# Kernel tuning notes

Hardware: AMD Instinct MI355X
Metric: run time of the kernel (lower is better)

## Reference

```python
import jax, jax.numpy as jnp
import numpy as np

E = 1024
H = 16
D = E // H
NUM_BUCKETS = 320
MAX_DISTANCE = 800


def _relative_positions_bucket(relative_positions):
    # relative_positions: int32 [T, S]
    num_buckets = NUM_BUCKETS // 2  # 160
    relative_buckets = (relative_positions > 0).astype(jnp.int32) * num_buckets
    rel = jnp.abs(relative_positions)
    max_exact = num_buckets // 2  # 80
    is_small = rel < max_exact
    rel_f = jnp.maximum(rel, 1).astype(jnp.float32)
    large = jnp.log(rel_f / max_exact) / np.log(MAX_DISTANCE / max_exact) * (num_buckets - max_exact)
    large = (max_exact + large).astype(jnp.int32)
    large = jnp.minimum(large, num_buckets - 1)
    relative_buckets = relative_buckets + jnp.where(is_small, rel, large)
    return relative_buckets


def setup_inputs() -> dict:
    key = jax.random.key(0)
    ks = jax.random.split(key, 12)
    B, T = 2, 2048
    s = 0.02
    return {
        "hidden_states": jax.random.normal(ks[0], (B, T, E), dtype=jnp.float32),
        "q_w": jax.random.normal(ks[1], (E, E), dtype=jnp.float32) * s,
        "q_b": jnp.zeros((E,), dtype=jnp.float32),
        "k_w": jax.random.normal(ks[2], (E, E), dtype=jnp.float32) * s,
        "k_b": jnp.zeros((E,), dtype=jnp.float32),
        "v_w": jax.random.normal(ks[3], (E, E), dtype=jnp.float32) * s,
        "v_b": jnp.zeros((E,), dtype=jnp.float32),
        "out_w": jax.random.normal(ks[4], (E, E), dtype=jnp.float32) * s,
        "out_b": jnp.zeros((E,), dtype=jnp.float32),
        "rel_embed": jax.random.normal(ks[5], (NUM_BUCKETS, H), dtype=jnp.float32) * s,
        "gru_const": jnp.ones((1, H, 1, 1), dtype=jnp.float32),
        "gru_w": jax.random.normal(ks[6], (8, D), dtype=jnp.float32) * s,
        "gru_b": jnp.zeros((8,), dtype=jnp.float32),
    }


def reference(hidden_states, q_w, q_b, k_w, k_b, v_w, v_b, out_w, out_b,
              rel_embed, gru_const, gru_w, gru_b):
    B, T, _ = hidden_states.shape
    scaling = D ** (-0.5)

    # --- relative position bias: [H, T, T] ---
    ctx = jnp.arange(T, dtype=jnp.int32)[:, None]
    mem = jnp.arange(T, dtype=jnp.int32)[None, :]
    buckets = _relative_positions_bucket(mem - ctx)          # [T, T]
    position_bias = rel_embed[buckets]                        # [T, T, H]
    position_bias = jnp.transpose(position_bias, (2, 0, 1))   # [H, T, T]

    # --- gate (gru_rel_pos): per (b, h, t) scalar ---
    gated = hidden_states.reshape(B, T, H, D).transpose(0, 2, 1, 3)  # [B,H,T,D]
    proj = jnp.einsum('bhtd,ed->bhte', gated, gru_w) + gru_b         # [B,H,T,8]
    proj = proj.reshape(B, H, T, 2, 4).sum(-1)                        # [B,H,T,2]
    gate = jax.nn.sigmoid(proj)
    gate_a = gate[..., 0:1]
    gate_b = gate[..., 1:2]
    gate_out = gate_a * (gate_b * gru_const - 1.0) + 2.0              # [B,H,T,1]
    gated_position_bias = gate_out * position_bias[None]              # [B,H,T,T]

    # --- attention (same math as F.multi_head_attention_forward eager path) ---
    q = (hidden_states @ q_w.T + q_b).reshape(B, T, H, D).transpose(0, 2, 1, 3) * scaling
    k = (hidden_states @ k_w.T + k_b).reshape(B, T, H, D).transpose(0, 2, 1, 3)
    v = (hidden_states @ v_w.T + v_b).reshape(B, T, H, D).transpose(0, 2, 1, 3)

    scores = jnp.einsum('bhtd,bhsd->bhts', q, k) + gated_position_bias
    attn = jax.nn.softmax(scores, axis=-1)
    ctx_out = jnp.einsum('bhts,bhsd->bhtd', attn, v)                  # [B,H,T,D]
    ctx_out = ctx_out.transpose(0, 2, 1, 3).reshape(B, T, E)
    return ctx_out @ out_w.T + out_b
```

## Files before the change

kernel.cpp:

```cpp
#include <hip/hip_runtime.h>
#include <hip/hip_bf16.h>
#include <math.h>

typedef __bf16 bf16;
typedef __bf16 bf16x4 __attribute__((ext_vector_type(4)));
typedef __bf16 bf16x8 __attribute__((ext_vector_type(8)));
typedef float  f32x4  __attribute__((ext_vector_type(4)));

#define T_SEQ 2048
#define E_DIM 1024
#define H_NUM 16
#define D_DIM 64
#define NDELTA 4095
#define LOG2E 1.4426950408889634f

__device__ __forceinline__ void gld16(const bf16* g, bf16* l) {
  __builtin_amdgcn_global_load_lds((__attribute__((address_space(1))) void*)(g),
                                   (__attribute__((address_space(3))) void*)(l), 16, 0, 0);
}

__global__ void cast_bf16_kernel(const float* __restrict__ src, bf16* __restrict__ dst, int n4) {
  int i = blockIdx.x * blockDim.x + threadIdx.x;
  if (i >= n4) return;
  const float4 v = reinterpret_cast<const float4*>(src)[i];
  bf16x4 o;
  o[0] = (bf16)v.x; o[1] = (bf16)v.y; o[2] = (bf16)v.z; o[3] = (bf16)v.w;
  reinterpret_cast<bf16x4*>(dst)[i] = o;
}

__global__ void cast_w_kernel(const float* __restrict__ q_w, const float* __restrict__ k_w,
                              const float* __restrict__ v_w, const float* __restrict__ o_w,
                              bf16* __restrict__ wcat, bf16* __restrict__ wob) {
  int i = blockIdx.x * 256 + threadIdx.x;
  int sel = blockIdx.y;
  const float* src = (sel == 0) ? q_w : (sel == 1) ? k_w : (sel == 2) ? v_w : o_w;
  bf16* dst = (sel < 3) ? (wcat + (size_t)sel * 1048576) : wob;
  const float4 v = reinterpret_cast<const float4*>(src)[i];
  bf16x4 o;
  o[0] = (bf16)v.x; o[1] = (bf16)v.y; o[2] = (bf16)v.z; o[3] = (bf16)v.w;
  reinterpret_cast<bf16x4*>(dst)[i] = o;
}

__global__ void pb_kernel(const float* __restrict__ rel_embed, float* __restrict__ pbt) {
  int dd = blockIdx.x * 64 + threadIdx.x;
  if (dd >= NDELTA) return;
  int delta = dd - (T_SEQ - 1);
  int bucket = (delta > 0) ? 160 : 0;
  int rel = abs(delta);
  int v;
  if (rel < 80) {
    v = rel;
  } else {
    float rf = (float)(rel < 1 ? 1 : rel);
    float lf = logf(rf / 80.0f) * (80.0f / 2.302585092994046f);
    int lg = 80 + (int)lf;
    v = lg < 159 ? lg : 159;
  }
  bucket += v;
#pragma unroll
  for (int h = 0; h < H_NUM; h++)
    pbt[h * NDELTA + dd] = rel_embed[bucket * H_NUM + h];
}

__global__ __launch_bounds__(256)
void gate_kernel(const float* __restrict__ hs, const float* __restrict__ gru_w,
                 const float* __restrict__ gru_b, const float* __restrict__ gconst,
                 float* __restrict__ gate)
{
  __shared__ float w[512];
  int tid = threadIdx.x;
  w[tid] = gru_w[tid];
  w[tid + 256] = gru_w[tid + 256];
  __syncthreads();
  int idx = blockIdx.x * 256 + tid;
  int h  = idx & 15;
  int bt = idx >> 4;
  const float* x = hs + (size_t)bt * E_DIM + h * D_DIM;
  float acc[8] = {0,0,0,0,0,0,0,0};
  for (int d = 0; d < 64; d += 4) {
    float4 xv = *(const float4*)&x[d];
#pragma unroll
    for (int e = 0; e < 8; e++) {
      acc[e] += xv.x * w[e*64+d] + xv.y * w[e*64+d+1]
              + xv.z * w[e*64+d+2] + xv.w * w[e*64+d+3];
    }
  }
  float p0 = acc[0]+acc[1]+acc[2]+acc[3] + gru_b[0]+gru_b[1]+gru_b[2]+gru_b[3];
  float p1 = acc[4]+acc[5]+acc[6]+acc[7] + gru_b[4]+gru_b[5]+gru_b[6]+gru_b[7];
  float ga = 1.0f / (1.0f + expf(-p0));
  float gb = 1.0f / (1.0f + expf(-p1));
  float g = (ga * (gb * gconst[h] - 1.0f) + 2.0f) * LOG2E;
  int bb = bt >> 11;
  int t  = bt & (T_SEQ - 1);
  gate[((size_t)(bb * H_NUM + h)) * T_SEQ + t] = g;
}

template<int MODE, int N_TOTAL>
__global__ __launch_bounds__(256)
void gemm2_kernel(const bf16* __restrict__ A, const bf16* __restrict__ W,
                  const float* __restrict__ b0, const float* __restrict__ b1,
                  const float* __restrict__ b2, float qalpha,
                  void* __restrict__ out0, void* __restrict__ out1, void* __restrict__ out2)
{
  __shared__ bf16 As[128 * 32];
  __shared__ bf16 Bs[128 * 32];
  const int tid  = threadIdx.x;
  const int lane = tid & 63;
  const int wave = tid >> 6;
  const int m0 = blockIdx.y * 128;
  const int n0 = blockIdx.x * 128;
  const int wm = (wave >> 1) * 64;
  const int wn = (wave & 1) * 64;
  const int qd = lane >> 4;
  const int lm = lane & 15;

  const int row4 = lane >> 2;
  const int col8 = (lane & 3) * 8;
  const bf16* gA0 = A + (size_t)(m0 + wave * 32 + row4) * 1024 + col8;
  const bf16* gA1 = gA0 + (size_t)16 * 1024;
  const bf16* gB0 = W + (size_t)(n0 + wave * 32 + row4) * 1024 + col8;
  const bf16* gB1 = gB0 + (size_t)16 * 1024;
  bf16* lA0 = As + (wave * 2 + 0) * 512;
  bf16* lA1 = As + (wave * 2 + 1) * 512;
  bf16* lB0 = Bs + (wave * 2 + 0) * 512;
  bf16* lB1 = Bs + (wave * 2 + 1) * 512;

  f32x4 acc[4][4] = {};

  for (int k0 = 0; k0 < 1024; k0 += 32) {
    gld16(gA0 + k0, lA0);
    gld16(gA1 + k0, lA1);
    gld16(gB0 + k0, lB0);
    gld16(gB1 + k0, lB1);
    __syncthreads();
    bf16x8 af[4], bfr[4];
#pragma unroll
    for (int i = 0; i < 4; i++) {
      af[i]  = *(const bf16x8*)&As[(wm + i * 16 + lm) * 32 + qd * 8];
      bfr[i] = *(const bf16x8*)&Bs[(wn + i * 16 + lm) * 32 + qd * 8];
    }
#pragma unroll
    for (int im = 0; im < 4; im++)
#pragma unroll
      for (int in = 0; in < 4; in++)
        acc[im][in] = __builtin_amdgcn_mfma_f32_16x16x32_bf16(af[im], bfr[in], acc[im][in], 0, 0, 0);
    __syncthreads();
  }

  const int seg = n0 >> 10;
  const float* bias = (MODE == 0) ? b0 : (seg == 0 ? b0 : (seg == 1 ? b1 : b2));
  const float alpha = (MODE == 1 && seg == 0) ? qalpha : 1.0f;

#pragma unroll
  for (int im = 0; im < 4; im++) {
#pragma unroll
    for (int in = 0; in < 4; in++) {
      const int n  = n0 + wn + in * 16 + lm;
      const int n1 = n & 1023;
      const float bv = bias[n1];
      const int mb = m0 + wm + im * 16 + qd * 4;
      if (MODE == 0) {
        float* o = (float*)out0;
#pragma unroll
        for (int r = 0; r < 4; r++)
          o[(size_t)(mb + r) * 1024 + n1] = acc[im][in][r] + bv;
      } else if (seg == 2) {
        const int bb = mb >> 11;
        const int t  = mb & 2047;
        bf16x4 pk;
#pragma unroll
        for (int r = 0; r < 4; r++) pk[r] = (bf16)(acc[im][in][r] + bv);
        *(bf16x4*)&((bf16*)out2)[((size_t)(bb * 1024 + n1)) * 2048 + t] = pk;
      } else {
        bf16* o = (bf16*)(seg == 0 ? out0 : out1);
#pragma unroll
        for (int r = 0; r < 4; r++)
          o[(size_t)(mb + r) * 1024 + n1] = (bf16)((acc[im][in][r] + bv) * alpha);
      }
    }
  }
}

#define LK 72
__global__ __launch_bounds__(256)
void attn3_kernel(const bf16* __restrict__ Qg, const bf16* __restrict__ Kg,
                  const bf16* __restrict__ Vtg, const float* __restrict__ gate,
                  const float* __restrict__ pbt, bf16* __restrict__ ctx)
{
  __shared__ bf16 Ks[2][64 * LK];
  __shared__ bf16 Vs[2][64 * LK];
  __shared__ bf16 Ps[4][32 * LK];
  __shared__ float pbs[2176];

  const int t0 = blockIdx.x * 128;
  const int h  = blockIdx.y;
  const int b  = blockIdx.z;
  const int tid  = threadIdx.x;
  const int lane = tid & 63;
  const int wave = tid >> 6;
  const int qd = lane >> 4;
  const int lm = lane & 15;

  for (int i = tid; i < 2176; i += 256) {
    int idx = i - t0 + 1920;
    pbs[i] = (idx >= 0 && idx < NDELTA) ? pbt[h * NDELTA + idx] : 0.0f;
  }

  bf16x8 qf[2][2];
  float g[2];
#pragma unroll
  for (int nb = 0; nb < 2; nb++) {
    const int q = t0 + wave * 32 + nb * 16 + lm;
    const bf16* qrow = Qg + (size_t)(b * T_SEQ + q) * E_DIM + h * D_DIM;
    qf[nb][0] = *(const bf16x8*)(qrow + qd * 8);
    qf[nb][1] = *(const bf16x8*)(qrow + 32 + qd * 8);
    g[nb] = gate[((size_t)(b * H_NUM + h)) * T_SEQ + q];
  }

  const int srow = tid >> 2;
  const int scol = (tid & 3) * 16;
  const bf16* kgp = Kg  + ((size_t)(b * T_SEQ) + srow) * E_DIM + h * D_DIM + scol;
  const bf16* vgp = Vtg + ((size_t)(b * 1024) + h * D_DIM + srow) * T_SEQ + scol;

  {
    bf16x8 a0 = *(const bf16x8*)kgp;
    bf16x8 a1 = *(const bf16x8*)(kgp + 8);
    bf16x8 c0 = *(const bf16x8*)vgp;
    bf16x8 c1 = *(const bf16x8*)(vgp + 8);
    *(bf16x8*)&Ks[0][srow * LK + scol]     = a0;
    *(bf16x8*)&Ks[0][srow * LK + scol + 8] = a1;
    *(bf16x8*)&Vs[0][srow * LK + scol]     = c0;
    *(bf16x8*)&Vs[0][srow * LK + scol + 8] = c1;
  }
  __syncthreads();

  f32x4 o[4][2] = {};
  float li[2] = {0.0f, 0.0f};
  bf16* psw = &Ps[wave][0];

  for (int it = 0; it < T_SEQ / 64; it++) {
    const int s0 = it * 64;
    const int buf = it & 1;
    const bool more = (it + 1 < T_SEQ / 64);
    bf16x8 nk0, nk1, nv0, nv1;
    if (more) {
      const bf16* kn = kgp + (size_t)(s0 + 64) * E_DIM;
      const bf16* vn = vgp + (s0 + 64);
      nk0 = *(const bf16x8*)kn; nk1 = *(const bf16x8*)(kn + 8);
      nv0 = *(const bf16x8*)vn; nv1 = *(const bf16x8*)(vn + 8);
    }

    bf16x8 kf[4][2];
#pragma unroll
    for (int mb = 0; mb < 4; mb++) {
      kf[mb][0] = *(const bf16x8*)&Ks[buf][(16 * mb + lm) * LK + qd * 8];
      kf[mb][1] = *(const bf16x8*)&Ks[buf][(16 * mb + lm) * LK + 32 + qd * 8];
    }
#pragma unroll
    for (int nb = 0; nb < 2; nb++) {
      f32x4 sc[4];
#pragma unroll
      for (int mb = 0; mb < 4; mb++) {
        f32x4 t = {};
        t = __builtin_amdgcn_mfma_f32_16x16x32_bf16(kf[mb][0], qf[nb][0], t, 0, 0, 0);
        t = __builtin_amdgcn_mfma_f32_16x16x32_bf16(kf[mb][1], qf[nb][1], t, 0, 0, 0);
        sc[mb] = t;
      }
      const int ib = s0 + 4 * qd + 127 - (wave * 32 + nb * 16 + lm);
      float rs = 0.0f;
#pragma unroll
      for (int mb = 0; mb < 4; mb++) {
        bf16x4 pk;
#pragma unroll
        for (int r = 0; r < 4; r++) {
          float p = __builtin_amdgcn_exp2f(sc[mb][r] + g[nb] * pbs[ib + 16 * mb + r]);
          rs += p;
          pk[r] = (bf16)p;
        }
        *(bf16x4*)&psw[(nb * 16 + lm) * LK + 16 * mb + 4 * qd] = pk;
      }
      li[nb] += rs;
    }
    bf16x8 pf[2][2];
#pragma unroll
    for (int nb = 0; nb < 2; nb++) {
      pf[nb][0] = *(const bf16x8*)&psw[(nb * 16 + lm) * LK + qd * 8];
      pf[nb][1] = *(const bf16x8*)&psw[(nb * 16 + lm) * LK + 32 + qd * 8];
    }
#pragma unroll
    for (int db = 0; db < 4; db++) {
      bf16x8 vf0 = *(const bf16x8*)&Vs[buf][(16 * db + lm) * LK + qd * 8];
      bf16x8 vf1 = *(const bf16x8*)&Vs[buf][(16 * db + lm) * LK + 32 + qd * 8];
#pragma unroll
      for (int nb = 0; nb < 2; nb++) {
        o[db][nb] = __builtin_amdgcn_mfma_f32_16x16x32_bf16(vf0, pf[nb][0], o[db][nb], 0, 0, 0);
        o[db][nb] = __builtin_amdgcn_mfma_f32_16x16x32_bf16(vf1, pf[nb][1], o[db][nb], 0, 0, 0);
      }
    }
    if (more) {
      *(bf16x8*)&Ks[buf ^ 1][srow * LK + scol]     = nk0;
      *(bf16x8*)&Ks[buf ^ 1][srow * LK + scol + 8] = nk1;
      *(bf16x8*)&Vs[buf ^ 1][srow * LK + scol]     = nv0;
      *(bf16x8*)&Vs[buf ^ 1][srow * LK + scol + 8] = nv1;
    }
    __syncthreads();
  }

#pragma unroll
  for (int nb = 0; nb < 2; nb++) {
    li[nb] += __shfl_xor(li[nb], 16);
    li[nb] += __shfl_xor(li[nb], 32);
  }
#pragma unroll
  for (int nb = 0; nb < 2; nb++) {
    const float inv = 1.0f / li[nb];
    const int q = t0 + wave * 32 + nb * 16 + lm;
    bf16* obase = ctx + (size_t)(b * T_SEQ + q) * E_DIM + h * D_DIM + 4 * qd;
#pragma unroll
    for (int db = 0; db < 4; db++) {
      bf16x4 ov;
      ov[0] = (bf16)(o[db][nb][0] * inv); ov[1] = (bf16)(o[db][nb][1] * inv);
      ov[2] = (bf16)(o[db][nb][2] * inv); ov[3] = (bf16)(o[db][nb][3] * inv);
      *(bf16x4*)&obase[16 * db] = ov;
    }
  }
}

extern "C" void kernel_launch(void* const* d_in, const int* in_sizes, int n_in,
                              void* d_out, int out_size, void* d_ws, size_t ws_size,
                              hipStream_t stream)
{
  const float* hs     = (const float*)d_in[0];
  const float* q_w    = (const float*)d_in[1];
  const float* q_b    = (const float*)d_in[2];
  const float* k_w    = (const float*)d_in[3];
  const float* k_b    = (const float*)d_in[4];
  const float* v_w    = (const float*)d_in[5];
  const float* v_b    = (const float*)d_in[6];
  const float* out_w  = (const float*)d_in[7];
  const float* out_b  = (const float*)d_in[8];
  const float* rel    = (const float*)d_in[9];
  const float* gconst = (const float*)d_in[10];
  const float* gru_w  = (const float*)d_in[11];
  const float* gru_b  = (const float*)d_in[12];

  char* p = (char*)d_ws;
  bf16* hsb  = (bf16*)p; p += (size_t)4096 * 1024 * 2;
  bf16* wcat = (bf16*)p; p += (size_t)3072 * 1024 * 2;
  bf16* wob  = (bf16*)p; p += (size_t)1024 * 1024 * 2;
  bf16* Qb   = (bf16*)p; p += (size_t)4096 * 1024 * 2;
  bf16* Kb   = (bf16*)p; p += (size_t)4096 * 1024 * 2;
  bf16* Vtb  = (bf16*)p; p += (size_t)2048 * 2048 * 2;
  bf16* ctxb = (bf16*)p; p += (size_t)4096 * 1024 * 2;
  float* gatep = (float*)p; p += (size_t)2 * H_NUM * T_SEQ * 4;
  float* pbt   = (float*)p; p += (size_t)H_NUM * NDELTA * 4;

  cast_bf16_kernel<<<4096, 256, 0, stream>>>(hs, hsb, 1048576);
  cast_w_kernel<<<dim3(1024, 4), 256, 0, stream>>>(q_w, k_w, v_w, out_w, wcat, wob);
  pb_kernel<<<64, 64, 0, stream>>>(rel, pbt);
  gate_kernel<<<256, 256, 0, stream>>>(hs, gru_w, gru_b, gconst, gatep);

  const float qalpha = 0.125f * LOG2E;
  gemm2_kernel<1, 3072><<<dim3(24, 32), 256, 0, stream>>>(
      hsb, wcat, q_b, k_b, v_b, qalpha, Qb, Kb, Vtb);

  attn3_kernel<<<dim3(T_SEQ / 128, H_NUM, 2), 256, 0, stream>>>(Qb, Kb, Vtb, gatep, pbt, ctxb);

  gemm2_kernel<0, 1024><<<dim3(8, 32), 256, 0, stream>>>(
      ctxb, wob, out_b, nullptr, nullptr, 1.0f, d_out, nullptr, nullptr);
}
```

Baseline: 227.8 us.

## Double-buffer GEMM LDS tiles and shrink tile sizes for more blocks

```diff
diff --git a/kernel.cpp b/kernel.cpp
--- a/kernel.cpp
+++ b/kernel.cpp
@@ -95,54 +95,63 @@
   gate[((size_t)(bb * H_NUM + h)) * T_SEQ + t] = g;
 }
 
-template<int MODE, int N_TOTAL>
-__global__ __launch_bounds__(256)
-void gemm2_kernel(const bf16* __restrict__ A, const bf16* __restrict__ W,
+template<int MODE, int BM, int BN>
+__global__ __launch_bounds__(256, 4)
+void gemm4_kernel(const bf16* __restrict__ A, const bf16* __restrict__ W,
                   const float* __restrict__ b0, const float* __restrict__ b1,
                   const float* __restrict__ b2, float qalpha,
                   void* __restrict__ out0, void* __restrict__ out1, void* __restrict__ out2)
 {
-  __shared__ bf16 As[128 * 32];
-  __shared__ bf16 Bs[128 * 32];
+  constexpr int AM = BM / 32;
+  constexpr int AN = BN / 32;
+  __shared__ bf16 As[2][BM * 32];
+  __shared__ bf16 Bs[2][BN * 32];
   const int tid  = threadIdx.x;
   const int lane = tid & 63;
   const int wave = tid >> 6;
-  const int m0 = blockIdx.y * 128;
-  const int n0 = blockIdx.x * 128;
-  const int wm = (wave >> 1) * 64;
-  const int wn = (wave & 1) * 64;
+  const int m0 = blockIdx.y * BM;
+  const int n0 = blockIdx.x * BN;
+  const int wm = (wave >> 1) * (BM / 2);
+  const int wn = (wave & 1) * (BN / 2);
   const int qd = lane >> 4;
   const int lm = lane & 15;
 
   const int row4 = lane >> 2;
   const int col8 = (lane & 3) * 8;
-  const bf16* gA0 = A + (size_t)(m0 + wave * 32 + row4) * 1024 + col8;
-  const bf16* gA1 = gA0 + (size_t)16 * 1024;
-  const bf16* gB0 = W + (size_t)(n0 + wave * 32 + row4) * 1024 + col8;
-  const bf16* gB1 = gB0 + (size_t)16 * 1024;
-  bf16* lA0 = As + (wave * 2 + 0) * 512;
-  bf16* lA1 = As + (wave * 2 + 1) * 512;
-  bf16* lB0 = Bs + (wave * 2 + 0) * 512;
-  bf16* lB1 = Bs + (wave * 2 + 1) * 512;
-
-  f32x4 acc[4][4] = {};
+  const bf16* gA0 = A + (size_t)(m0 + wave * (BM / 4) + row4) * 1024 + col8;
+  const bf16* gB0 = W + (size_t)(n0 + wave * (BN / 4) + row4) * 1024 + col8;
+  bf16* lA = (bf16*)As + wave * (BM / 4) * 32;
+  bf16* lB = (bf16*)Bs + wave * (BN / 4) * 32;
+
+  gld16(gA0, lA);
+  if (BM == 128) gld16(gA0 + (size_t)16 * 1024, lA + 512);
+  gld16(gB0, lB);
+  if (BN == 128) gld16(gB0 + (size_t)16 * 1024, lB + 512);
+  __syncthreads();
+
+  f32x4 acc[AM][AN] = {};
 
   for (int k0 = 0; k0 < 1024; k0 += 32) {
-    gld16(gA0 + k0, lA0);
-    gld16(gA1 + k0, lA1);
-    gld16(gB0 + k0, lB0);
-    gld16(gB1 + k0, lB1);
-    __syncthreads();
-    bf16x8 af[4], bfr[4];
-#pragma unroll
-    for (int i = 0; i < 4; i++) {
-      af[i]  = *(const bf16x8*)&As[(wm + i * 16 + lm) * 32 + qd * 8];
-      bfr[i] = *(const bf16x8*)&Bs[(wn + i * 16 + lm) * 32 + qd * 8];
-    }
-#pragma unroll
-    for (int im = 0; im < 4; im++)
-#pragma unroll
-      for (int in = 0; in < 4; in++)
+    const int buf = (k0 >> 5) & 1;
+    if (k0 + 32 < 1024) {
+      bf16* lA1 = lA + (buf ^ 1) * (BM * 32);
+      bf16* lB1 = lB + (buf ^ 1) * (BN * 32);
+      gld16(gA0 + k0 + 32, lA1);
+      if (BM == 128) gld16(gA0 + (size_t)16 * 1024 + k0 + 32, lA1 + 512);
+      gld16(gB0 + k0 + 32, lB1);
+      if (BN == 128) gld16(gB0 + (size_t)16 * 1024 + k0 + 32, lB1 + 512);
+    }
+    bf16x8 af[AM], bfr[AN];
+#pragma unroll
+    for (int i = 0; i < AM; i++)
+      af[i]  = *(const bf16x8*)&As[buf][(wm + i * 16 + lm) * 32 + qd * 8];
+#pragma unroll
+    for (int i = 0; i < AN; i++)
+      bfr[i] = *(const bf16x8*)&Bs[buf][(wn + i * 16 + lm) * 32 + qd * 8];
+#pragma unroll
+    for (int im = 0; im < AM; im++)
+#pragma unroll
+      for (int in = 0; in < AN; in++)
         acc[im][in] = __builtin_amdgcn_mfma_f32_16x16x32_bf16(af[im], bfr[in], acc[im][in], 0, 0, 0);
     __syncthreads();
   }
@@ -152,9 +161,9 @@
   const float alpha = (MODE == 1 && seg == 0) ? qalpha : 1.0f;
 
 #pragma unroll
-  for (int im = 0; im < 4; im++) {
-#pragma unroll
-    for (int in = 0; in < 4; in++) {
+  for (int im = 0; im < AM; im++) {
+#pragma unroll
+    for (int in = 0; in < AN; in++) {
       const int n  = n0 + wn + in * 16 + lm;
       const int n1 = n & 1023;
       const float bv = bias[n1];
@@ -361,11 +370,11 @@
   gate_kernel<<<256, 256, 0, stream>>>(hs, gru_w, gru_b, gconst, gatep);
 
   const float qalpha = 0.125f * LOG2E;
-  gemm2_kernel<1, 3072><<<dim3(24, 32), 256, 0, stream>>>(
+  gemm4_kernel<1, 64, 128><<<dim3(24, 64), 256, 0, stream>>>(
       hsb, wcat, q_b, k_b, v_b, qalpha, Qb, Kb, Vtb);
 
   attn3_kernel<<<dim3(T_SEQ / 128, H_NUM, 2), 256, 0, stream>>>(Qb, Kb, Vtb, gatep, pbt, ctxb);
 
-  gemm2_kernel<0, 1024><<<dim3(8, 32), 256, 0, stream>>>(
+  gemm4_kernel<0, 64, 64><<<dim3(16, 64), 256, 0, stream>>>(
       ctxb, wob, out_b, nullptr, nullptr, 1.0f, d_out, nullptr, nullptr);
 }
```

After: 229.9 us. Within noise of the previous version (+0.9%).
